# Optimization experiments

Hardware: AMD Instinct MI355X
Metric: run time of the kernel (lower is better)

Reference implementation:

```python
import jax, jax.numpy as jnp
import numpy as np

B, C, H, W = 4, 256, 64, 64
TOPK = 3
RAT_S = 0.05  # rat_s passed in Corr.forward


def _zero_window_mask(h, w, rat_s=RAT_S):
    # mask[m, i, j] = 1 - gaussian centered at pixel m=(m//w, m%w); sigma=(h*rat_s, w*rat_s)
    sr, sc = h * rat_s, w * rat_s
    r = jnp.arange(h, dtype=jnp.float32)
    c = jnp.arange(w, dtype=jnp.float32)
    cent_r = jnp.repeat(r, w)  # [hw]
    cent_c = jnp.tile(c, h)    # [hw]
    g = (jnp.exp(-((r[None, :, None] - cent_r[:, None, None]) ** 2) / (2.0 * sr * sr))
         * jnp.exp(-((c[None, None, :] - cent_c[:, None, None]) ** 2) / (2.0 * sc * sc)))
    return (1.0 - g).reshape(h * w, h * w)


def setup_inputs() -> dict:
    key = jax.random.key(0)
    x = jax.random.normal(key, (B, C, H, W), dtype=jnp.float32)
    alpha = jnp.asarray(5.0, dtype=jnp.float32)  # learned scalar nn.Parameter
    return {"x": x, "alpha": alpha}


def reference(x, alpha):
    b, c, h, w = x.shape
    # F.normalize(x, p=2, dim=-3): L2-normalize channels with eps clamp
    nrm = jnp.linalg.norm(x, axis=1, keepdims=True)
    xn = x / jnp.maximum(nrm, 1e-12)
    xf = xn.reshape(b, c, h * w)
    # correlation GEMM: [b, hw, hw]
    aff = jnp.einsum('bcm,bcn->bmn', xf, xf)
    aff = aff * _zero_window_mask(h, w)[None]
    s = aff * alpha
    xc = jax.nn.softmax(s, axis=-1) * jax.nn.softmax(s, axis=-2)
    # topk over the source-pixel dim (dim=-3 of [b, hw, h, w])
    xc = xc.reshape(b, h * w, h, w).transpose(0, 2, 3, 1)  # [b, h, w, hw]
    val, _ = jax.lax.top_k(xc, TOPK)                        # [b, h, w, k]
    return val.transpose(0, 3, 1, 2)                        # [b, k, h, w]
```

## Files before the change

kernel.cpp:

```cpp
#include <hip/hip_runtime.h>
#include <hip/hip_bf16.h>
#include <math.h>


#define HW 4096
#define CDIM 256
#define INV2S2 0.048828125f
#define NEGINF -1e30f
#define NTILE 528
#define LOG2E 1.4426950408889634f

#if defined(__has_builtin)
#  if __has_builtin(__builtin_amdgcn_exp2f)
#    define EXP2F(x) __builtin_amdgcn_exp2f(x)
#  else
#    define EXP2F(x) exp2f(x)
#  endif
#else
#  define EXP2F(x) exp2f(x)
#endif

typedef __bf16 bf16;
typedef _Float16 f16;
typedef __attribute__((ext_vector_type(8))) __bf16 bf16x8;
typedef __attribute__((ext_vector_type(4))) _Float16 f16x4;
typedef __attribute__((ext_vector_type(4))) float f32x4;

#define GAS __attribute__((address_space(1)))
#define LAS __attribute__((address_space(3)))

__device__ __forceinline__ void ins3(float v, float& t0, float& t1, float& t2) {
    float n0 = fmaxf(t0, v);
    float n1 = __builtin_amdgcn_fmed3f(t0, t1, v);
    float n2 = __builtin_amdgcn_fmed3f(t1, t2, v);
    t0 = n0; t1 = n1; t2 = n2;
}

__device__ __forceinline__ void decode_tri(int t, int& mt, int& nt) {
    int m = (int)((sqrtf(8.f * (float)t + 1.f) - 1.f) * 0.5f);
    while ((m + 1) * (m + 2) / 2 <= t) ++m;
    while (m * (m + 1) / 2 > t) --m;
    mt = m;
    nt = t - m * (m + 1) / 2;
}

__global__ __launch_bounds__(256) void corr_norm(const float* __restrict__ x,
                                                 bf16* __restrict__ xnT) {
    __shared__ float red[4][64];
    __shared__ float invn[64];
    __shared__ __align__(16) bf16 T[64][264];
    int tid = threadIdx.x;
    int pl = tid & 63, cg = tid >> 6;
    int P0 = blockIdx.x * 64;
    int P = P0 + pl;
    int b = P >> 12;
    int pix = P & 4095;
    const float* xb = x + ((size_t)(b * CDIM + cg * 64) << 12) + pix;
    float v[64];
    float ss = 0.f;
#pragma unroll
    for (int j = 0; j < 64; ++j) {
        v[j] = xb[(size_t)j << 12];
        ss += v[j] * v[j];
    }
    red[cg][pl] = ss;
    __syncthreads();
    if (tid < 64) {
        float s = red[0][tid] + red[1][tid] + red[2][tid] + red[3][tid];
        invn[tid] = 1.0f / fmaxf(sqrtf(s), 1e-12f);
    }
    __syncthreads();
    float inv = invn[pl];
#pragma unroll
    for (int j0 = 0; j0 < 64; j0 += 8) {
        bf16x8 pk;
#pragma unroll
        for (int j = 0; j < 8; ++j) pk[j] = (bf16)(v[j0 + j] * inv);
        *(bf16x8*)(&T[pl][cg * 64 + j0]) = pk;
    }
    __syncthreads();
#pragma unroll
    for (int it = 0; it < 8; ++it) {
        int p = it * 8 + (tid >> 5);
        int k = tid & 31;
        bf16x8 val = *(const bf16x8*)(&T[p][k * 8]);
        *(bf16x8*)(xnT + (size_t)(P0 + p) * CDIM + k * 8) = val;
    }
}

__device__ __forceinline__ void build_ext(float* extw, int lane, int adr, float scale) {
    float fr2 = (float)(adr * adr);
#pragma unroll
    for (int h = 0; h < 2; ++h) {
        int j = lane + h * 64;
        float d = (float)(j - 63);
        extw[j] = scale * (1.f - __expf(-(fr2 + d * d) * INV2S2));
    }
}

__device__ __forceinline__ void load_etab(const float* extw_wave, int quad, int l15,
                                          float (&e)[7][4]) {
    const float* p = extw_wave + 63 + quad * 4 - l15;
#pragma unroll
    for (int dm = 0; dm < 7; ++dm)
#pragma unroll
        for (int r = 0; r < 4; ++r) e[dm][r] = p[(dm - 3) * 16 + r];
}

__global__ __launch_bounds__(256) void corr_rowsum(const bf16* __restrict__ xnT,
                                                   const float* __restrict__ alpha_p,
                                                   float* __restrict__ rpart,
                                                   f16* __restrict__ sbuf,
                                                   int store_s2) {
    __shared__ __align__(16) bf16 SH[12288];
    bf16* As = SH;
    bf16* Bs = SH + 4096;
    int tid = threadIdx.x;
    int lin = blockIdx.x;
    int xcd = lin & 7;
    int b = xcd >> 1;
    int v = lin >> 3;
    int h = v & 1;
    int t = ((v >> 1) << 1) + (xcd & 1);
    int mt, nt;
    decode_tri(t, mt, nt);
    int mbase = mt * 128 + h * 64;
    int nbase = nt * 128;
    int wave = tid >> 6, lane = tid & 63;
    int wm = wave >> 1, wn = wave & 1, l15 = lane & 15, quad = lane >> 4;
    int rowi = mbase >> 6;
    int coli = (nbase + wn * 64) >> 6;
    int adr = rowi - coli; if (adr < 0) adr = -adr;
    float alpha2 = alpha_p[0] * LOG2E;
    const bf16* xb = xnT + ((size_t)b << 20);
    const int rslot = ((quad + (l15 >> 1)) & 3) * 8;

    auto issue = [&](int kk, int buf) {
        {
            int idx = tid;
            int prow = idx >> 2;
            int sub = ((idx & 3) - (prow >> 1)) & 3;
            const bf16* gA = xb + ((size_t)(mbase + prow) << 8) + kk * 32 + (sub << 3);
            bf16* lA = As + buf * 2048 + (wave << 9);
            __builtin_amdgcn_global_load_lds((const GAS void*)gA, (LAS void*)lA, 16, 0, 0);
        }
#pragma unroll
        for (int r = 0; r < 2; ++r) {
            int idx = r * 256 + tid;
            int prow = idx >> 2;
            int sub = ((idx & 3) - (prow >> 1)) & 3;
            const bf16* gB = xb + ((size_t)(nbase + prow) << 8) + kk * 32 + (sub << 3);
            bf16* lB = Bs + buf * 4096 + ((r * 4 + wave) << 9);
            __builtin_amdgcn_global_load_lds((const GAS void*)gB, (LAS void*)lB, 16, 0, 0);
        }
    };

    f32x4 acc[2][4];
#pragma unroll
    for (int mi = 0; mi < 2; ++mi)
#pragma unroll
        for (int ni = 0; ni < 4; ++ni) acc[mi][ni] = (f32x4)0.f;

    issue(0, 0);
#pragma unroll
    for (int kk = 0; kk < 8; ++kk) {
        __syncthreads();
        if (kk < 7) issue(kk + 1, (kk + 1) & 1);
        int buf = kk & 1;
        bf16x8 af[2], bfr[4];
#pragma unroll
        for (int i = 0; i < 2; ++i)
            af[i] = *(const bf16x8*)(As + buf * 2048 + (wm * 32 + i * 16 + l15) * 32 + rslot);
#pragma unroll
        for (int i = 0; i < 4; ++i)
            bfr[i] = *(const bf16x8*)(Bs + buf * 4096 + (wn * 64 + i * 16 + l15) * 32 + rslot);
#pragma unroll
        for (int mi = 0; mi < 2; ++mi)
#pragma unroll
            for (int ni = 0; ni < 4; ++ni)
                acc[mi][ni] = __builtin_amdgcn_mfma_f32_16x16x32_bf16(af[mi], bfr[ni],
                                                                      acc[mi][ni], 0, 0, 0);
    }

    float* F = (float*)SH;
    float* ext  = F;
    float* rbuf = F + 512;
    float* cbuf = F + 640;
    build_ext(ext + wave * 128, lane, adr, alpha2);
    float e[5][4];
    {
        const float* p = ext + wave * 128 + 63 + wm * 32 + quad * 4 - l15;
#pragma unroll
        for (int dm = 0; dm < 5; ++dm)
#pragma unroll
            for (int r = 0; r < 4; ++r) e[dm][r] = p[(dm - 3) * 16 + r];
    }

    const size_t tb = (size_t)(b * NTILE + t) * 16384;
    float colpart[4] = {0.f, 0.f, 0.f, 0.f};
#pragma unroll
    for (int mi = 0; mi < 2; ++mi) {
#pragma unroll
        for (int r = 0; r < 4; ++r) {
            float ssum = 0.f;
            float sv[4];
#pragma unroll
            for (int ni = 0; ni < 4; ++ni) {
                float p = e[mi - ni + 3][r] * acc[mi][ni][r];
                sv[ni] = p;
                float ev = EXP2F(p);
                ssum += ev;
                colpart[ni] += ev;
            }
            if (store_s2) {
                f16x4 pk;
#pragma unroll
                for (int ni = 0; ni < 4; ++ni) pk[ni] = (f16)(sv[ni] + sv[ni]);
                *(f16x4*)(sbuf + tb + ((wm * 2 + mi) * 4 + r) * 1024 +
                          ((h * 2 + wn) * 64 + lane) * 4) = pk;
            }
            ssum += __shfl_xor(ssum, 1);
            ssum += __shfl_xor(ssum, 2);
            ssum += __shfl_xor(ssum, 4);
            ssum += __shfl_xor(ssum, 8);
            if (l15 == 0) rbuf[wn * 64 + wm * 32 + mi * 16 + quad * 4 + r] = ssum;
        }
    }
#pragma unroll
    for (int ni = 0; ni < 4; ++ni) {
        float c = colpart[ni];
        c += __shfl_xor(c, 16);
        c += __shfl_xor(c, 32);
        if (quad == 0) cbuf[wm * 128 + wn * 64 + ni * 16 + l15] = c;
    }
    __syncthreads();
    if (tid < 128) {
        int j = tid;
        float vr = ((j >> 6) == h) ? (rbuf[j & 63] + rbuf[64 + (j & 63)]) : 0.f;
        rpart[(size_t)((b * 32 + mt) * 64 + nt * 2 + h) * 128 + j] = vr;
    } else if (mt != nt) {
        int j = tid - 128;
        rpart[(size_t)((b * 32 + nt) * 64 + mt * 2 + h) * 128 + j] = cbuf[j] + cbuf[128 + j];
    }
}

__global__ __launch_bounds__(256) void corr_recip(const float* __restrict__ rpart,
                                                  float* __restrict__ ism,
                                                  float* __restrict__ lsm) {
    int i = blockIdx.x * 256 + threadIdx.x;
    if (i >= 4 * HW) return;
    int b = i >> 12, gr = i & 4095, s = gr >> 7, j = gr & 127;
    const float* base = rpart + (size_t)((b * 32 + s) * 64) * 128 + j;
    float sum = 0.f;
#pragma unroll
    for (int sl = 0; sl < 64; ++sl) sum += base[sl * 128];
    ism[i] = 1.0f / sum;
    lsm[i] = -log2f(sum);
}

__device__ __forceinline__ void topk_epilogue(int b, int mt, int nt,
                                              const float (&s2f)[16][4],
                                              const float (&lr)[4][4], const float (&lc)[4],
                                              float* mbuf, float* rtop,
                                              float* __restrict__ wtop,
                                              int tid, int wm, int wn, int l15, int quad) {
#pragma unroll
    for (int ni = 0; ni < 4; ++ni) {
        float t0 = NEGINF, t1 = NEGINF, t2 = NEGINF;
#pragma unroll
        for (int mi = 0; mi < 4; ++mi) {
#pragma unroll
            for (int r = 0; r < 4; ++r) {
                float key = s2f[mi * 4 + r][ni] + lr[mi][r];
                ins3(key, t0, t1, t2);
            }
        }
#pragma unroll
        for (int d = 16; d <= 32; d <<= 1) {
            float s0 = __shfl_xor(t0, d);
            float s1 = __shfl_xor(t1, d);
            float s2 = __shfl_xor(t2, d);
            ins3(s0, t0, t1, t2);
            ins3(s1, t0, t1, t2);
            ins3(s2, t0, t1, t2);
        }
        if (quad == 0) {
            int cl = wn * 64 + ni * 16 + l15;
            mbuf[(wm * 128 + cl) * 3 + 0] = t0;
            mbuf[(wm * 128 + cl) * 3 + 1] = t1;
            mbuf[(wm * 128 + cl) * 3 + 2] = t2;
        }
    }
    __syncthreads();
    if (mt != nt) {
#pragma unroll
        for (int mi = 0; mi < 4; ++mi) {
#pragma unroll
            for (int r = 0; r < 4; ++r) {
                float u0 = NEGINF, u1 = NEGINF, u2 = NEGINF;
#pragma unroll
                for (int ni = 0; ni < 4; ++ni) {
                    float key = s2f[mi * 4 + r][ni] + lc[ni];
                    ins3(key, u0, u1, u2);
                }
                {
                    float s0 = __shfl_xor(u0, 8);
                    float s1 = __shfl_xor(u1, 8);
                    float s2 = __shfl_xor(u2, 8);
                    ins3(s0, u0, u1, u2);
                    ins3(s1, u0, u1, u2);
                    ins3(s2, u0, u1, u2);
                }
                if (l15 < 8) {
                    int row = wm * 64 + mi * 16 + quad * 4 + r;
                    int slot = wn * 8 + l15;
                    float* q = rtop + row * 51 + slot * 3;
                    q[0] = u0; q[1] = u1; q[2] = u2;
                }
            }
        }
    }
    __syncthreads();
    if (tid < 128) {
        float t0 = mbuf[tid * 3], t1 = mbuf[tid * 3 + 1], t2 = mbuf[tid * 3 + 2];
        ins3(mbuf[(128 + tid) * 3 + 0], t0, t1, t2);
        ins3(mbuf[(128 + tid) * 3 + 1], t0, t1, t2);
        ins3(mbuf[(128 + tid) * 3 + 2], t0, t1, t2);
        size_t o = ((size_t)((b * 32 + nt) * 32 + mt) * 128 + tid) * 3;
        wtop[o] = t0;
        wtop[o + 1] = t1;
        wtop[o + 2] = t2;
        if (mt != nt) {
            float v0 = NEGINF, v1 = NEGINF, v2 = NEGINF;
            const float* q = rtop + tid * 51;
#pragma unroll
            for (int sl = 0; sl < 16; ++sl) {
                ins3(q[sl * 3 + 0], v0, v1, v2);
                ins3(q[sl * 3 + 1], v0, v1, v2);
                ins3(q[sl * 3 + 2], v0, v1, v2);
            }
            size_t o2 = ((size_t)((b * 32 + mt) * 32 + nt) * 128 + tid) * 3;
            wtop[o2] = v0;
            wtop[o2 + 1] = v1;
            wtop[o2 + 2] = v2;
        }
    }
}

__global__ __launch_bounds__(256) void corr_topsel(const f16* __restrict__ sbuf,
                                                   const float* __restrict__ lsm,
                                                   float* __restrict__ wtop) {
    __shared__ float FS[7296];
    float* mbuf = FS;
    float* rtop = FS + 768;
    int tid = threadIdx.x;
    int lin = blockIdx.x;
    int xcd = lin & 7;
    int b = xcd >> 1;
    int t = ((lin >> 3) << 1) + (xcd & 1);
    int mt, nt;
    decode_tri(t, mt, nt);
    int mbase = mt * 128, nbase = nt * 128;
    int wave = tid >> 6, lane = tid & 63;
    int wm = wave >> 1, wn = wave & 1, l15 = lane & 15, quad = lane >> 4;

    const size_t tb = (size_t)(b * NTILE + t) * 16384;
    float s2f[16][4];
#pragma unroll
    for (int k = 0; k < 16; ++k) {
        f16x4 hv = __builtin_nontemporal_load((const f16x4*)(sbuf + tb + k * 1024 + tid * 4));
#pragma unroll
        for (int ni = 0; ni < 4; ++ni) s2f[k][ni] = (float)hv[ni];
    }
    float lr[4][4];
#pragma unroll
    for (int mi = 0; mi < 4; ++mi)
#pragma unroll
        for (int r = 0; r < 4; ++r)
            lr[mi][r] = lsm[(b << 12) + mbase + wm * 64 + mi * 16 + quad * 4 + r];
    float lc[4];
#pragma unroll
    for (int ni = 0; ni < 4; ++ni)
        lc[ni] = lsm[(b << 12) + nbase + wn * 64 + ni * 16 + l15];

    topk_epilogue(b, mt, nt, s2f, lr, lc, mbuf, rtop, wtop, tid, wm, wn, l15, quad);
}

__global__ __launch_bounds__(256) void corr_topk(const bf16* __restrict__ xnT,
                                                 const float* __restrict__ alpha_p,
                                                 const float* __restrict__ lsm,
                                                 float* __restrict__ wtop) {
    __shared__ __align__(16) bf16 SH[16384];
    bf16* As = SH;
    bf16* Bs = SH + 8192;
    int tid = threadIdx.x;
    int lin = blockIdx.x;
    int xcd = lin & 7;
    int b = xcd >> 1;
    int t = ((lin >> 3) << 1) + (xcd & 1);
    int mt, nt;
    decode_tri(t, mt, nt);
    int mbase = mt * 128, nbase = nt * 128;
    int wave = tid >> 6, lane = tid & 63;
    int wm = wave >> 1, wn = wave & 1, l15 = lane & 15, quad = lane >> 4;
    int rowi = (mbase + wm * 64) >> 6;
    int coli = (nbase + wn * 64) >> 6;
    int adr = rowi - coli; if (adr < 0) adr = -adr;
    float a2 = 2.0f * alpha_p[0] * LOG2E;
    const bf16* xb = xnT + ((size_t)b << 20);
    const int rslot = ((quad + (l15 >> 1)) & 3) * 8;

    auto issue = [&](int kk, int buf) {
#pragma unroll
        for (int r = 0; r < 2; ++r) {
            int idx = r * 256 + tid;
            int prow = idx >> 2;
            int sub = ((idx & 3) - (prow >> 1)) & 3;
            const bf16* gA = xb + ((size_t)(mbase + prow) << 8) + kk * 32 + (sub << 3);
            const bf16* gB = xb + ((size_t)(nbase + prow) << 8) + kk * 32 + (sub << 3);
            bf16* lA = As + buf * 4096 + ((r * 4 + wave) << 9);
            bf16* lB = Bs + buf * 4096 + ((r * 4 + wave) << 9);
            __builtin_amdgcn_global_load_lds((const GAS void*)gA, (LAS void*)lA, 16, 0, 0);
            __builtin_amdgcn_global_load_lds((const GAS void*)gB, (LAS void*)lB, 16, 0, 0);
        }
    };

    f32x4 acc[4][4];
#pragma unroll
    for (int mi = 0; mi < 4; ++mi)
#pragma unroll
        for (int ni = 0; ni < 4; ++ni) acc[mi][ni] = (f32x4)0.f;
    issue(0, 0);
#pragma unroll
    for (int kk = 0; kk < 8; ++kk) {
        __syncthreads();
        if (kk < 7) issue(kk + 1, (kk + 1) & 1);
        int buf = kk & 1;
        bf16x8 af[4], bfr[4];
#pragma unroll
        for (int i = 0; i < 4; ++i) {
            af[i]  = *(const bf16x8*)(As + buf * 4096 + (wm * 64 + i * 16 + l15) * 32 + rslot);
            bfr[i] = *(const bf16x8*)(Bs + buf * 4096 + (wn * 64 + i * 16 + l15) * 32 + rslot);
        }
#pragma unroll
        for (int mi = 0; mi < 4; ++mi)
#pragma unroll
            for (int ni = 0; ni < 4; ++ni)
                acc[mi][ni] = __builtin_amdgcn_mfma_f32_16x16x32_bf16(af[mi], bfr[ni],
                                                                      acc[mi][ni], 0, 0, 0);
    }

    float* Fh = (float*)SH;
    float* ext  = Fh;
    float* mbuf = Fh + 512;
    float* rtop = Fh + 1280;
    build_ext(ext + wave * 128, lane, adr, a2);
    float e[7][4];
    load_etab(ext + wave * 128, quad, l15, e);

    float s2f[16][4];
#pragma unroll
    for (int mi = 0; mi < 4; ++mi)
#pragma unroll
        for (int r = 0; r < 4; ++r)
#pragma unroll
            for (int ni = 0; ni < 4; ++ni)
                s2f[mi * 4 + r][ni] = e[mi - ni + 3][r] * acc[mi][ni][r];
    float lr[4][4];
#pragma unroll
    for (int mi = 0; mi < 4; ++mi)
#pragma unroll
        for (int r = 0; r < 4; ++r)
            lr[mi][r] = lsm[(b << 12) + mbase + wm * 64 + mi * 16 + quad * 4 + r];
    float lc[4];
#pragma unroll
    for (int ni = 0; ni < 4; ++ni)
        lc[ni] = lsm[(b << 12) + nbase + wn * 64 + ni * 16 + l15];

    __syncthreads();
    topk_epilogue(b, mt, nt, s2f, lr, lc, mbuf, rtop, wtop, tid, wm, wn, l15, quad);
}

__global__ __launch_bounds__(256) void corr_merge(const float* __restrict__ wtop,
                                                  const float* __restrict__ ism,
                                                  float* __restrict__ out) {
    int idx = blockIdx.x * 256 + threadIdx.x;
    if (idx >= 4 * HW) return;
    int b = idx >> 12, col = idx & 4095;
    int strip = col >> 7, j = col & 127;
    const float* base = wtop + ((size_t)((b * 32 + strip) * 32) * 128 + j) * 3;
    float t0 = NEGINF, t1 = NEGINF, t2 = NEGINF;
    for (int sl = 0; sl < 32; ++sl) {
        const float* q = base + (size_t)sl * 128 * 3;
        ins3(q[0], t0, t1, t2);
        ins3(q[1], t0, t1, t2);
        ins3(q[2], t0, t1, t2);
    }
    float ismc = ism[idx];
    out[((b * 3 + 0) << 12) + col] = EXP2F(t0) * ismc;
    out[((b * 3 + 1) << 12) + col] = EXP2F(t1) * ismc;
    out[((b * 3 + 2) << 12) + col] = EXP2F(t2) * ismc;
}

extern "C" void kernel_launch(void* const* d_in, const int* in_sizes, int n_in,
                              void* d_out, int out_size, void* d_ws, size_t ws_size,
                              hipStream_t stream) {
    const float* x = (const float*)d_in[0];
    const float* alpha = (const float*)d_in[1];
    float* out = (float*)d_out;
    char* ws = (char*)d_ws;
    bf16* xnT = (bf16*)ws;
    float* ism = (float*)(ws + (8u << 20));
    float* lsm = (float*)(ws + (8u << 20) + (64u << 10));
    float* rpart = (float*)(ws + (8u << 20) + (128u << 10));
    float* wtop  = (float*)(ws + (8u << 20) + (128u << 10));
    f16* sbuf = (f16*)(ws + (8u << 20) + (128u << 10) + (6u << 20));
    size_t need = (8u << 20) + (128u << 10) + (6u << 20) + (size_t)4 * NTILE * 16384 * 2;
    int fast = (ws_size >= need);

    corr_norm<<<256, 256, 0, stream>>>(x, xnT);
    corr_rowsum<<<NTILE * 8, 256, 0, stream>>>(xnT, alpha, rpart, sbuf, fast);
    corr_recip<<<64, 256, 0, stream>>>(rpart, ism, lsm);
    if (fast)
        corr_topsel<<<NTILE * 4, 256, 0, stream>>>(sbuf, lsm, wtop);
    else
        corr_topk<<<NTILE * 4, 256, 0, stream>>>(xnT, alpha, lsm, wtop);
    corr_merge<<<64, 256, 0, stream>>>(wtop, ism, out);
}
```

Measured before the change: 131.4 us.

## Split rowsum GEMM tiles into 64x64 quarter blocks with finer partial sums

The row/column softmax-sum kernel now processes 64x64 sub-tiles instead of 64x128. That doubles the grid, cuts LDS per block and drops accumulator registers from 8 to 4 per thread. Each wave handles one 16-row strip against all 64 columns, and the partial-sum buffer is re-laid out as 64x64 slots, with the reciprocal kernel updated to match. The aim is higher occupancy and better latency hiding, at the cost of less operand reuse per block and more redundant global loads.

```diff
diff --git a/kernel.cpp b/kernel.cpp
--- a/kernel.cpp
+++ b/kernel.cpp
@@ -112,135 +112,117 @@
                                                    float* __restrict__ rpart,
                                                    f16* __restrict__ sbuf,
                                                    int store_s2) {
-    __shared__ __align__(16) bf16 SH[12288];
+    __shared__ __align__(16) bf16 SH[8192];
     bf16* As = SH;
     bf16* Bs = SH + 4096;
     int tid = threadIdx.x;
     int lin = blockIdx.x;
     int xcd = lin & 7;
     int b = xcd >> 1;
-    int v = lin >> 3;
-    int h = v & 1;
-    int t = ((v >> 1) << 1) + (xcd & 1);
+    int u = lin >> 3;
+    int qv = u & 3;
+    int hr = qv >> 1, hc = qv & 1;
+    int t = ((u >> 2) << 1) + (xcd & 1);
     int mt, nt;
     decode_tri(t, mt, nt);
-    int mbase = mt * 128 + h * 64;
-    int nbase = nt * 128;
+    int mbase = mt * 128 + hr * 64;
+    int nbase = nt * 128 + hc * 64;
+    int ms = mt * 2 + hr, ns = nt * 2 + hc;
     int wave = tid >> 6, lane = tid & 63;
-    int wm = wave >> 1, wn = wave & 1, l15 = lane & 15, quad = lane >> 4;
-    int rowi = mbase >> 6;
-    int coli = (nbase + wn * 64) >> 6;
-    int adr = rowi - coli; if (adr < 0) adr = -adr;
+    int l15 = lane & 15, quad = lane >> 4;
+    int adr = ms - ns; if (adr < 0) adr = -adr;
     float alpha2 = alpha_p[0] * LOG2E;
     const bf16* xb = xnT + ((size_t)b << 20);
     const int rslot = ((quad + (l15 >> 1)) & 3) * 8;
 
     auto issue = [&](int kk, int buf) {
-        {
-            int idx = tid;
-            int prow = idx >> 2;
-            int sub = ((idx & 3) - (prow >> 1)) & 3;
-            const bf16* gA = xb + ((size_t)(mbase + prow) << 8) + kk * 32 + (sub << 3);
-            bf16* lA = As + buf * 2048 + (wave << 9);
-            __builtin_amdgcn_global_load_lds((const GAS void*)gA, (LAS void*)lA, 16, 0, 0);
-        }
-#pragma unroll
-        for (int r = 0; r < 2; ++r) {
-            int idx = r * 256 + tid;
-            int prow = idx >> 2;
-            int sub = ((idx & 3) - (prow >> 1)) & 3;
-            const bf16* gB = xb + ((size_t)(nbase + prow) << 8) + kk * 32 + (sub << 3);
-            bf16* lB = Bs + buf * 4096 + ((r * 4 + wave) << 9);
-            __builtin_amdgcn_global_load_lds((const GAS void*)gB, (LAS void*)lB, 16, 0, 0);
-        }
+        int prow = tid >> 2;
+        int sub = ((tid & 3) - (prow >> 1)) & 3;
+        const bf16* gA = xb + ((size_t)(mbase + prow) << 8) + kk * 32 + (sub << 3);
+        const bf16* gB = xb + ((size_t)(nbase + prow) << 8) + kk * 32 + (sub << 3);
+        bf16* lA = As + buf * 2048 + (wave << 9);
+        bf16* lB = Bs + buf * 2048 + (wave << 9);
+        __builtin_amdgcn_global_load_lds((const GAS void*)gA, (LAS void*)lA, 16, 0, 0);
+        __builtin_amdgcn_global_load_lds((const GAS void*)gB, (LAS void*)lB, 16, 0, 0);
     };
 
-    f32x4 acc[2][4];
-#pragma unroll
-    for (int mi = 0; mi < 2; ++mi)
-#pragma unroll
-        for (int ni = 0; ni < 4; ++ni) acc[mi][ni] = (f32x4)0.f;
-
+    f32x4 acc[4];
+#pragma unroll
+    for (int ni = 0; ni < 4; ++ni) acc[ni] = (f32x4)0.f;
     issue(0, 0);
 #pragma unroll
     for (int kk = 0; kk < 8; ++kk) {
         __syncthreads();
         if (kk < 7) issue(kk + 1, (kk + 1) & 1);
         int buf = kk & 1;
-        bf16x8 af[2], bfr[4];
-#pragma unroll
-        for (int i = 0; i < 2; ++i)
-            af[i] = *(const bf16x8*)(As + buf * 2048 + (wm * 32 + i * 16 + l15) * 32 + rslot);
+        bf16x8 af = *(const bf16x8*)(As + buf * 2048 + (wave * 16 + l15) * 32 + rslot);
+        bf16x8 bfr[4];
 #pragma unroll
         for (int i = 0; i < 4; ++i)
-            bfr[i] = *(const bf16x8*)(Bs + buf * 4096 + (wn * 64 + i * 16 + l15) * 32 + rslot);
-#pragma unroll
-        for (int mi = 0; mi < 2; ++mi)
-#pragma unroll
-            for (int ni = 0; ni < 4; ++ni)
-                acc[mi][ni] = __builtin_amdgcn_mfma_f32_16x16x32_bf16(af[mi], bfr[ni],
-                                                                      acc[mi][ni], 0, 0, 0);
+            bfr[i] = *(const bf16x8*)(Bs + buf * 2048 + (i * 16 + l15) * 32 + rslot);
+#pragma unroll
+        for (int ni = 0; ni < 4; ++ni)
+            acc[ni] = __builtin_amdgcn_mfma_f32_16x16x32_bf16(af, bfr[ni], acc[ni], 0, 0, 0);
     }
 
     float* F = (float*)SH;
     float* ext  = F;
     float* rbuf = F + 512;
-    float* cbuf = F + 640;
+    float* cbuf = F + 576;
     build_ext(ext + wave * 128, lane, adr, alpha2);
-    float e[5][4];
+    float e[4][4];
     {
-        const float* p = ext + wave * 128 + 63 + wm * 32 + quad * 4 - l15;
-#pragma unroll
-        for (int dm = 0; dm < 5; ++dm)
-#pragma unroll
-            for (int r = 0; r < 4; ++r) e[dm][r] = p[(dm - 3) * 16 + r];
+        const float* p = ext + wave * 128 + 63 + wave * 16 + quad * 4 - l15;
+#pragma unroll
+        for (int ni = 0; ni < 4; ++ni)
+#pragma unroll
+            for (int r = 0; r < 4; ++r) e[ni][r] = p[r - ni * 16];
     }
 
     const size_t tb = (size_t)(b * NTILE + t) * 16384;
     float colpart[4] = {0.f, 0.f, 0.f, 0.f};
 #pragma unroll
-    for (int mi = 0; mi < 2; ++mi) {
-#pragma unroll
-        for (int r = 0; r < 4; ++r) {
-            float ssum = 0.f;
-            float sv[4];
-#pragma unroll
-            for (int ni = 0; ni < 4; ++ni) {
-                float p = e[mi - ni + 3][r] * acc[mi][ni][r];
-                sv[ni] = p;
-                float ev = EXP2F(p);
-                ssum += ev;
-                colpart[ni] += ev;
-            }
-            if (store_s2) {
-                f16x4 pk;
-#pragma unroll
-                for (int ni = 0; ni < 4; ++ni) pk[ni] = (f16)(sv[ni] + sv[ni]);
-                *(f16x4*)(sbuf + tb + ((wm * 2 + mi) * 4 + r) * 1024 +
-                          ((h * 2 + wn) * 64 + lane) * 4) = pk;
-            }
-            ssum += __shfl_xor(ssum, 1);
-            ssum += __shfl_xor(ssum, 2);
-            ssum += __shfl_xor(ssum, 4);
-            ssum += __shfl_xor(ssum, 8);
-            if (l15 == 0) rbuf[wn * 64 + wm * 32 + mi * 16 + quad * 4 + r] = ssum;
-        }
+    for (int r = 0; r < 4; ++r) {
+        float ssum = 0.f;
+        float sv[4];
+#pragma unroll
+        for (int ni = 0; ni < 4; ++ni) {
+            float pp = e[ni][r] * acc[ni][r];
+            sv[ni] = pp;
+            float ev = EXP2F(pp);
+            ssum += ev;
+            colpart[ni] += ev;
+        }
+        if (store_s2) {
+            f16x4 pk;
+#pragma unroll
+            for (int ni = 0; ni < 4; ++ni) pk[ni] = (f16)(sv[ni] + sv[ni]);
+            *(f16x4*)(sbuf + tb + (wave * 4 + r) * 1024 +
+                      (((hr * 2 + hc) * 64 + lane) << 2)) = pk;
+        }
+        ssum += __shfl_xor(ssum, 1);
+        ssum += __shfl_xor(ssum, 2);
+        ssum += __shfl_xor(ssum, 4);
+        ssum += __shfl_xor(ssum, 8);
+        if (l15 == 0) rbuf[wave * 16 + quad * 4 + r] = ssum;
     }
 #pragma unroll
     for (int ni = 0; ni < 4; ++ni) {
         float c = colpart[ni];
         c += __shfl_xor(c, 16);
         c += __shfl_xor(c, 32);
-        if (quad == 0) cbuf[wm * 128 + wn * 64 + ni * 16 + l15] = c;
-    }
-    __syncthreads();
-    if (tid < 128) {
-        int j = tid;
-        float vr = ((j >> 6) == h) ? (rbuf[j & 63] + rbuf[64 + (j & 63)]) : 0.f;
-        rpart[(size_t)((b * 32 + mt) * 64 + nt * 2 + h) * 128 + j] = vr;
-    } else if (mt != nt) {
-        int j = tid - 128;
-        rpart[(size_t)((b * 32 + nt) * 64 + mt * 2 + h) * 128 + j] = cbuf[j] + cbuf[128 + j];
+        if (quad == 0) cbuf[wave * 64 + ni * 16 + l15] = c;
+    }
+    __syncthreads();
+    bool skiprp = (mt == nt) && (hr == 0) && (hc == 1);
+    if (!skiprp) {
+        if (tid < 64) {
+            rpart[((size_t)(b * 64 + ms) * 64 + ns) * 64 + tid] = rbuf[tid];
+        } else if (tid < 128 && ms != ns) {
+            int j = tid - 64;
+            rpart[((size_t)(b * 64 + ns) * 64 + ms) * 64 + j] =
+                cbuf[j] + cbuf[64 + j] + cbuf[128 + j] + cbuf[192 + j];
+        }
     }
 }
 
@@ -249,11 +231,11 @@
                                                   float* __restrict__ lsm) {
     int i = blockIdx.x * 256 + threadIdx.x;
     if (i >= 4 * HW) return;
-    int b = i >> 12, gr = i & 4095, s = gr >> 7, j = gr & 127;
-    const float* base = rpart + (size_t)((b * 32 + s) * 64) * 128 + j;
+    int b = i >> 12, gr = i & 4095, s = gr >> 6, j = gr & 63;
+    const float* base = rpart + ((size_t)(b * 64 + s) * 64) * 64 + j;
     float sum = 0.f;
 #pragma unroll
-    for (int sl = 0; sl < 64; ++sl) sum += base[sl * 128];
+    for (int sl = 0; sl < 64; ++sl) sum += base[sl * 64];
     ism[i] = 1.0f / sum;
     lsm[i] = -log2f(sum);
 }
@@ -519,7 +501,7 @@
     int fast = (ws_size >= need);
 
     corr_norm<<<256, 256, 0, stream>>>(x, xnT);
-    corr_rowsum<<<NTILE * 8, 256, 0, stream>>>(xnT, alpha, rpart, sbuf, fast);
+    corr_rowsum<<<NTILE * 16, 256, 0, stream>>>(xnT, alpha, rpart, sbuf, fast);
     corr_recip<<<64, 256, 0, stream>>>(rpart, ism, lsm);
     if (fast)
         corr_topsel<<<NTILE * 4, 256, 0, stream>>>(sbuf, lsm, wtop);
```

Result: slower. 134.5 us (+2.3%).

## Split top-k selection tiles into half-tile blocks and double merge slots

Applied to the files above, without the earlier changes.

The top-k selection kernel now launches twice as many blocks, each handling half of a 128x128 tile's rows. This cuts per-thread register use (8 rows instead of 16) and shared memory (4032 floats instead of 7296), which should raise occupancy and parallelism. The partial-result buffer is widened to 64 slots per strip, with unused slots filled with -inf, and the workspace layout is reshuffled so wtop can overlay xnT in the fast path. The cost is that the final merge kernel reads twice as many partial entries, and more blocks redo lsm loads.

```diff
diff --git a/kernel.cpp b/kernel.cpp
--- a/kernel.cpp
+++ b/kernel.cpp
@@ -258,23 +258,53 @@
     lsm[i] = -log2f(sum);
 }
 
-__device__ __forceinline__ void topk_epilogue(int b, int mt, int nt,
-                                              const float (&s2f)[16][4],
-                                              const float (&lr)[4][4], const float (&lc)[4],
-                                              float* mbuf, float* rtop,
-                                              float* __restrict__ wtop,
-                                              int tid, int wm, int wn, int l15, int quad) {
+__global__ __launch_bounds__(256) void corr_topsel(const f16* __restrict__ sbuf,
+                                                   const float* __restrict__ lsm,
+                                                   float* __restrict__ wtop) {
+    __shared__ float FS[4032];
+    float* mbuf = FS;
+    float* rtop = FS + 768;
+    int tid = threadIdx.x;
+    int lin = blockIdx.x;
+    int xcd = lin & 7;
+    int b = xcd >> 1;
+    int u = lin >> 3;
+    int h = u & 1;
+    int t = ((u >> 1) << 1) + (xcd & 1);
+    int mt, nt;
+    decode_tri(t, mt, nt);
+    int z = tid >> 7;
+    int sl = tid & 127;
+    int wn = (sl >> 6) & 1, lane = sl & 63;
+    int l15 = lane & 15, quad = lane >> 4;
+
+    const size_t tb = (size_t)(b * NTILE + t) * 16384;
+    float s2f[8][4];
+#pragma unroll
+    for (int kk = 0; kk < 8; ++kk) {
+        int k = z * 8 + kk;
+        f16x4 hv = __builtin_nontemporal_load(
+            (const f16x4*)(sbuf + tb + k * 1024 + (h * 128 + sl) * 4));
+#pragma unroll
+        for (int ni = 0; ni < 4; ++ni) s2f[kk][ni] = (float)hv[ni];
+    }
+    float lr[8];
+#pragma unroll
+    for (int kk = 0; kk < 8; ++kk) {
+        int rowin = h * 64 + (z * 2 + (kk >> 2)) * 16 + quad * 4 + (kk & 3);
+        lr[kk] = lsm[(b << 12) + mt * 128 + rowin];
+    }
+    float lc[4];
+#pragma unroll
+    for (int ni = 0; ni < 4; ++ni)
+        lc[ni] = lsm[(b << 12) + nt * 128 + wn * 64 + ni * 16 + l15];
+
 #pragma unroll
     for (int ni = 0; ni < 4; ++ni) {
         float t0 = NEGINF, t1 = NEGINF, t2 = NEGINF;
 #pragma unroll
-        for (int mi = 0; mi < 4; ++mi) {
-#pragma unroll
-            for (int r = 0; r < 4; ++r) {
-                float key = s2f[mi * 4 + r][ni] + lr[mi][r];
-                ins3(key, t0, t1, t2);
-            }
-        }
+        for (int kk = 0; kk < 8; ++kk)
+            ins3(s2f[kk][ni] + lr[kk], t0, t1, t2);
 #pragma unroll
         for (int d = 16; d <= 32; d <<= 1) {
             float s0 = __shfl_xor(t0, d);
@@ -286,37 +316,32 @@
         }
         if (quad == 0) {
             int cl = wn * 64 + ni * 16 + l15;
-            mbuf[(wm * 128 + cl) * 3 + 0] = t0;
-            mbuf[(wm * 128 + cl) * 3 + 1] = t1;
-            mbuf[(wm * 128 + cl) * 3 + 2] = t2;
+            mbuf[(z * 128 + cl) * 3 + 0] = t0;
+            mbuf[(z * 128 + cl) * 3 + 1] = t1;
+            mbuf[(z * 128 + cl) * 3 + 2] = t2;
         }
     }
     __syncthreads();
     if (mt != nt) {
 #pragma unroll
-        for (int mi = 0; mi < 4; ++mi) {
-#pragma unroll
-            for (int r = 0; r < 4; ++r) {
-                float u0 = NEGINF, u1 = NEGINF, u2 = NEGINF;
-#pragma unroll
-                for (int ni = 0; ni < 4; ++ni) {
-                    float key = s2f[mi * 4 + r][ni] + lc[ni];
-                    ins3(key, u0, u1, u2);
-                }
-                {
-                    float s0 = __shfl_xor(u0, 8);
-                    float s1 = __shfl_xor(u1, 8);
-                    float s2 = __shfl_xor(u2, 8);
-                    ins3(s0, u0, u1, u2);
-                    ins3(s1, u0, u1, u2);
-                    ins3(s2, u0, u1, u2);
-                }
-                if (l15 < 8) {
-                    int row = wm * 64 + mi * 16 + quad * 4 + r;
-                    int slot = wn * 8 + l15;
-                    float* q = rtop + row * 51 + slot * 3;
-                    q[0] = u0; q[1] = u1; q[2] = u2;
-                }
+        for (int kk = 0; kk < 8; ++kk) {
+            float u0 = NEGINF, u1 = NEGINF, u2 = NEGINF;
+#pragma unroll
+            for (int ni = 0; ni < 4; ++ni)
+                ins3(s2f[kk][ni] + lc[ni], u0, u1, u2);
+            {
+                float s0 = __shfl_xor(u0, 8);
+                float s1 = __shfl_xor(u1, 8);
+                float s2 = __shfl_xor(u2, 8);
+                ins3(s0, u0, u1, u2);
+                ins3(s1, u0, u1, u2);
+                ins3(s2, u0, u1, u2);
+            }
+            if (l15 < 8) {
+                int rloc = z * 32 + (kk >> 2) * 16 + quad * 4 + (kk & 3);
+                int slot = wn * 8 + l15;
+                float* q = rtop + rloc * 51 + slot * 3;
+                q[0] = u0; q[1] = u1; q[2] = u2;
             }
         }
     }
@@ -326,64 +351,30 @@
         ins3(mbuf[(128 + tid) * 3 + 0], t0, t1, t2);
         ins3(mbuf[(128 + tid) * 3 + 1], t0, t1, t2);
         ins3(mbuf[(128 + tid) * 3 + 2], t0, t1, t2);
-        size_t o = ((size_t)((b * 32 + nt) * 32 + mt) * 128 + tid) * 3;
+        size_t o = ((size_t)((b * 32 + nt) * 64 + 2 * mt + h) * 128 + tid) * 3;
         wtop[o] = t0;
         wtop[o + 1] = t1;
         wtop[o + 2] = t2;
-        if (mt != nt) {
-            float v0 = NEGINF, v1 = NEGINF, v2 = NEGINF;
-            const float* q = rtop + tid * 51;
-#pragma unroll
-            for (int sl = 0; sl < 16; ++sl) {
-                ins3(q[sl * 3 + 0], v0, v1, v2);
-                ins3(q[sl * 3 + 1], v0, v1, v2);
-                ins3(q[sl * 3 + 2], v0, v1, v2);
-            }
-            size_t o2 = ((size_t)((b * 32 + mt) * 32 + nt) * 128 + tid) * 3;
-            wtop[o2] = v0;
-            wtop[o2 + 1] = v1;
-            wtop[o2 + 2] = v2;
-        }
-    }
-}
-
-__global__ __launch_bounds__(256) void corr_topsel(const f16* __restrict__ sbuf,
-                                                   const float* __restrict__ lsm,
-                                                   float* __restrict__ wtop) {
-    __shared__ float FS[7296];
-    float* mbuf = FS;
-    float* rtop = FS + 768;
-    int tid = threadIdx.x;
-    int lin = blockIdx.x;
-    int xcd = lin & 7;
-    int b = xcd >> 1;
-    int t = ((lin >> 3) << 1) + (xcd & 1);
-    int mt, nt;
-    decode_tri(t, mt, nt);
-    int mbase = mt * 128, nbase = nt * 128;
-    int wave = tid >> 6, lane = tid & 63;
-    int wm = wave >> 1, wn = wave & 1, l15 = lane & 15, quad = lane >> 4;
-
-    const size_t tb = (size_t)(b * NTILE + t) * 16384;
-    float s2f[16][4];
-#pragma unroll
-    for (int k = 0; k < 16; ++k) {
-        f16x4 hv = __builtin_nontemporal_load((const f16x4*)(sbuf + tb + k * 1024 + tid * 4));
-#pragma unroll
-        for (int ni = 0; ni < 4; ++ni) s2f[k][ni] = (float)hv[ni];
-    }
-    float lr[4][4];
-#pragma unroll
-    for (int mi = 0; mi < 4; ++mi)
-#pragma unroll
-        for (int r = 0; r < 4; ++r)
-            lr[mi][r] = lsm[(b << 12) + mbase + wm * 64 + mi * 16 + quad * 4 + r];
-    float lc[4];
-#pragma unroll
-    for (int ni = 0; ni < 4; ++ni)
-        lc[ni] = lsm[(b << 12) + nbase + wn * 64 + ni * 16 + l15];
-
-    topk_epilogue(b, mt, nt, s2f, lr, lc, mbuf, rtop, wtop, tid, wm, wn, l15, quad);
+    }
+    if (mt != nt && tid < 64) {
+        float v0 = NEGINF, v1 = NEGINF, v2 = NEGINF;
+        const float* q = rtop + tid * 51;
+#pragma unroll
+        for (int sls = 0; sls < 16; ++sls) {
+            ins3(q[sls * 3 + 0], v0, v1, v2);
+            ins3(q[sls * 3 + 1], v0, v1, v2);
+            ins3(q[sls * 3 + 2], v0, v1, v2);
+        }
+        int jg = h * 64 + tid;
+        size_t o2 = ((size_t)((b * 32 + mt) * 64 + 2 * nt) * 128 + jg) * 3;
+        wtop[o2] = v0;
+        wtop[o2 + 1] = v1;
+        wtop[o2 + 2] = v2;
+        size_t o3 = ((size_t)((b * 32 + mt) * 64 + 2 * nt + 1) * 128 + jg) * 3;
+        wtop[o3] = NEGINF;
+        wtop[o3 + 1] = NEGINF;
+        wtop[o3 + 2] = NEGINF;
+    }
 }
 
 __global__ __launch_bounds__(256) void corr_topk(const bf16* __restrict__ xnT,
@@ -478,7 +469,91 @@
         lc[ni] = lsm[(b << 12) + nbase + wn * 64 + ni * 16 + l15];
 
     __syncthreads();
-    topk_epilogue(b, mt, nt, s2f, lr, lc, mbuf, rtop, wtop, tid, wm, wn, l15, quad);
+
+#pragma unroll
+    for (int ni = 0; ni < 4; ++ni) {
+        float t0 = NEGINF, t1 = NEGINF, t2 = NEGINF;
+#pragma unroll
+        for (int mi = 0; mi < 4; ++mi)
+#pragma unroll
+            for (int r = 0; r < 4; ++r)
+                ins3(s2f[mi * 4 + r][ni] + lr[mi][r], t0, t1, t2);
+#pragma unroll
+        for (int d = 16; d <= 32; d <<= 1) {
+            float s0 = __shfl_xor(t0, d);
+            float s1 = __shfl_xor(t1, d);
+            float s2 = __shfl_xor(t2, d);
+            ins3(s0, t0, t1, t2);
+            ins3(s1, t0, t1, t2);
+            ins3(s2, t0, t1, t2);
+        }
+        if (quad == 0) {
+            int cl = wn * 64 + ni * 16 + l15;
+            mbuf[(wm * 128 + cl) * 3 + 0] = t0;
+            mbuf[(wm * 128 + cl) * 3 + 1] = t1;
+            mbuf[(wm * 128 + cl) * 3 + 2] = t2;
+        }
+    }
+    __syncthreads();
+    if (mt != nt) {
+#pragma unroll
+        for (int mi = 0; mi < 4; ++mi) {
+#pragma unroll
+            for (int r = 0; r < 4; ++r) {
+                float u0 = NEGINF, u1 = NEGINF, u2 = NEGINF;
+#pragma unroll
+                for (int ni = 0; ni < 4; ++ni)
+                    ins3(s2f[mi * 4 + r][ni] + lc[ni], u0, u1, u2);
+                {
+                    float s0 = __shfl_xor(u0, 8);
+                    float s1 = __shfl_xor(u1, 8);
+                    float s2 = __shfl_xor(u2, 8);
+                    ins3(s0, u0, u1, u2);
+                    ins3(s1, u0, u1, u2);
+                    ins3(s2, u0, u1, u2);
+                }
+                if (l15 < 8) {
+                    int row = wm * 64 + mi * 16 + quad * 4 + r;
+                    int slot = wn * 8 + l15;
+                    float* q = rtop + row * 51 + slot * 3;
+                    q[0] = u0; q[1] = u1; q[2] = u2;
+                }
+            }
+        }
+    }
+    __syncthreads();
+    if (tid < 128) {
+        float t0 = mbuf[tid * 3], t1 = mbuf[tid * 3 + 1], t2 = mbuf[tid * 3 + 2];
+        ins3(mbuf[(128 + tid) * 3 + 0], t0, t1, t2);
+        ins3(mbuf[(128 + tid) * 3 + 1], t0, t1, t2);
+        ins3(mbuf[(128 + tid) * 3 + 2], t0, t1, t2);
+        size_t o = ((size_t)((b * 32 + nt) * 64 + 2 * mt) * 128 + tid) * 3;
+        wtop[o] = t0;
+        wtop[o + 1] = t1;
+        wtop[o + 2] = t2;
+        size_t oz = ((size_t)((b * 32 + nt) * 64 + 2 * mt + 1) * 128 + tid) * 3;
+        wtop[oz] = NEGINF;
+        wtop[oz + 1] = NEGINF;
+        wtop[oz + 2] = NEGINF;
+        if (mt != nt) {
+            float v0 = NEGINF, v1 = NEGINF, v2 = NEGINF;
+            const float* q = rtop + tid * 51;
+#pragma unroll
+            for (int sls = 0; sls < 16; ++sls) {
+                ins3(q[sls * 3 + 0], v0, v1, v2);
+                ins3(q[sls * 3 + 1], v0, v1, v2);
+                ins3(q[sls * 3 + 2], v0, v1, v2);
+            }
+            size_t o2 = ((size_t)((b * 32 + mt) * 64 + 2 * nt) * 128 + tid) * 3;
+            wtop[o2] = v0;
+            wtop[o2 + 1] = v1;
+            wtop[o2 + 2] = v2;
+            size_t o3 = ((size_t)((b * 32 + mt) * 64 + 2 * nt + 1) * 128 + tid) * 3;
+            wtop[o3] = NEGINF;
+            wtop[o3 + 1] = NEGINF;
+            wtop[o3 + 2] = NEGINF;
+        }
+    }
 }
 
 __global__ __launch_bounds__(256) void corr_merge(const float* __restrict__ wtop,
@@ -488,9 +563,9 @@
     if (idx >= 4 * HW) return;
     int b = idx >> 12, col = idx & 4095;
     int strip = col >> 7, j = col & 127;
-    const float* base = wtop + ((size_t)((b * 32 + strip) * 32) * 128 + j) * 3;
+    const float* base = wtop + ((size_t)((b * 32 + strip) * 64) * 128 + j) * 3;
     float t0 = NEGINF, t1 = NEGINF, t2 = NEGINF;
-    for (int sl = 0; sl < 32; ++sl) {
+    for (int sl = 0; sl < 64; ++sl) {
         const float* q = base + (size_t)sl * 128 * 3;
         ins3(q[0], t0, t1, t2);
         ins3(q[1], t0, t1, t2);
@@ -509,20 +584,23 @@
     const float* alpha = (const float*)d_in[1];
     float* out = (float*)d_out;
     char* ws = (char*)d_ws;
+    const size_t SB = (size_t)4 * NTILE * 16384 * 2;
+    const size_t M12 = 12u << 20;
     bf16* xnT = (bf16*)ws;
-    float* ism = (float*)(ws + (8u << 20));
-    float* lsm = (float*)(ws + (8u << 20) + (64u << 10));
-    float* rpart = (float*)(ws + (8u << 20) + (128u << 10));
-    float* wtop  = (float*)(ws + (8u << 20) + (128u << 10));
-    f16* sbuf = (f16*)(ws + (8u << 20) + (128u << 10) + (6u << 20));
-    size_t need = (8u << 20) + (128u << 10) + (6u << 20) + (size_t)4 * NTILE * 16384 * 2;
-    int fast = (ws_size >= need);
+    float* rpart = (float*)(ws + (8u << 20));
+    f16* sbuf = (f16*)(ws + M12);
+    size_t need_fast = M12 + SB + (128u << 10);
+    int fast = (ws_size >= need_fast);
+    float* wtop = fast ? (float*)ws : (float*)(ws + M12);
+    char* tail = fast ? (ws + M12 + SB) : (ws + M12 + M12);
+    float* ism = (float*)tail;
+    float* lsm = (float*)(tail + (64u << 10));
 
     corr_norm<<<256, 256, 0, stream>>>(x, xnT);
     corr_rowsum<<<NTILE * 8, 256, 0, stream>>>(xnT, alpha, rpart, sbuf, fast);
     corr_recip<<<64, 256, 0, stream>>>(rpart, ism, lsm);
     if (fast)
-        corr_topsel<<<NTILE * 4, 256, 0, stream>>>(sbuf, lsm, wtop);
+        corr_topsel<<<NTILE * 8, 256, 0, stream>>>(sbuf, lsm, wtop);
     else
         corr_topk<<<NTILE * 4, 256, 0, stream>>>(xnT, alpha, lsm, wtop);
     corr_merge<<<64, 256, 0, stream>>>(wtop, ism, out);
```

New measurement: 139.0 us. +5.8%, slower.
